# Optimization experiments

Hardware: AMD Instinct MI355X
Metric: run time of the kernel (lower is better)

## Reference

```python
import jax, jax.numpy as jnp
import numpy as np

HEADS = 8
HID = 128
N_A = 10000
N_B = 10000
E = 120000
NG = 8  # graphs in batch
F_A = 256
F_B = 128
NEG_SLOPE = 0.2


def _gat(h_src, h_dst, src, dst, ws, wd, a_s, a_d, bias, num_dst):
    """PyG GATConv, bipartite, concat=False, add_self_loops=False."""
    hs = (h_src @ ws).reshape(-1, HEADS, HID)   # [N_src, H, C]
    hd = (h_dst @ wd).reshape(-1, HEADS, HID)   # [N_dst, H, C]
    al_s = jnp.sum(hs * a_s, axis=-1)           # [N_src, H]
    al_d = jnp.sum(hd * a_d, axis=-1)           # [N_dst, H]
    e = jax.nn.leaky_relu(al_s[src] + al_d[dst], NEG_SLOPE)  # [E, H]
    m = jax.ops.segment_max(e, dst, num_segments=num_dst)
    ex = jnp.exp(e - m[dst])
    denom = jax.ops.segment_sum(ex, dst, num_segments=num_dst)
    alpha = ex / (denom[dst] + 1e-16)           # segment softmax over in-edges
    msg = hs[src] * alpha[:, :, None]           # [E, H, C]
    out = jax.ops.segment_sum(msg, dst, num_segments=num_dst)
    return out.mean(axis=1) + bias              # concat=False -> head mean + bias


def _mean_pool(x, batch, num_graphs):
    s = jax.ops.segment_sum(x, batch, num_segments=num_graphs)
    cnt = jax.ops.segment_sum(jnp.ones((x.shape[0],), x.dtype), batch, num_segments=num_graphs)
    return s / jnp.maximum(cnt, 1.0)[:, None]


def setup_inputs() -> dict:
    key = jax.random.key(0)
    ks = iter(jax.random.split(key, 48))
    rn = lambda shape, s=0.05: jax.random.normal(next(ks), shape, jnp.float32) * s
    inp = {
        'x_a': jax.random.normal(next(ks), (N_A, F_A), jnp.float32),
        'x_b': jax.random.normal(next(ks), (N_B, F_B), jnp.float32),
        'edge_ab': jax.random.randint(next(ks), (2, E), 0, N_A, jnp.int32),
        'edge_ba': jax.random.randint(next(ks), (2, E), 0, N_B, jnp.int32),
        'batch_a': jnp.sort(jax.random.randint(next(ks), (N_A,), 0, NG, jnp.int32)),
        'batch_b': jnp.sort(jax.random.randint(next(ks), (N_B,), 0, NG, jnp.int32)),
        'lin_a_w': rn((F_A, HID)), 'lin_a_b': rn((HID,)),
        'lin_b_w': rn((F_B, HID)), 'lin_b_b': rn((HID,)),
        'fc_w': rn((2 * HID, 1)), 'fc_b': rn((1,)),
    }
    for layer in ('1', '2'):
        for rel in ('ab', 'ba'):
            inp[f'w{layer}s_{rel}'] = rn((HID, HEADS * HID))
            inp[f'w{layer}d_{rel}'] = rn((HID, HEADS * HID))
            inp[f'a{layer}s_{rel}'] = rn((HEADS, HID))
            inp[f'a{layer}d_{rel}'] = rn((HEADS, HID))
            inp[f'b{layer}_{rel}'] = rn((HID,))
    return inp


def reference(x_a, x_b, edge_ab, edge_ba, batch_a, batch_b,
              lin_a_w, lin_a_b, lin_b_w, lin_b_b, fc_w, fc_b,
              w1s_ab, w1d_ab, a1s_ab, a1d_ab, b1_ab,
              w1s_ba, w1d_ba, a1s_ba, a1d_ba, b1_ba,
              w2s_ab, w2d_ab, a2s_ab, a2d_ab, b2_ab,
              w2s_ba, w2d_ba, a2s_ba, a2d_ba, b2_ba):
    ha = jax.nn.relu(x_a @ lin_a_w + lin_a_b)
    hb = jax.nn.relu(x_b @ lin_b_w + lin_b_b)
    # layer 1 (each dst type receives exactly one relation -> HeteroConv mean is identity)
    hb1 = _gat(ha, hb, edge_ab[0], edge_ab[1], w1s_ab, w1d_ab, a1s_ab, a1d_ab, b1_ab, N_B)
    ha1 = _gat(hb, ha, edge_ba[0], edge_ba[1], w1s_ba, w1d_ba, a1s_ba, a1d_ba, b1_ba, N_A)
    ha1 = jax.nn.relu(ha1)
    hb1 = jax.nn.relu(hb1)
    # layer 2
    hb2 = _gat(ha1, hb1, edge_ab[0], edge_ab[1], w2s_ab, w2d_ab, a2s_ab, a2d_ab, b2_ab, N_B)
    ha2 = _gat(hb1, ha1, edge_ba[0], edge_ba[1], w2s_ba, w2d_ba, a2s_ba, a2d_ba, b2_ba, N_A)
    pa = _mean_pool(ha2, batch_a, NG)
    pb = _mean_pool(hb2, batch_b, NG)
    g = jnp.concatenate([pa, pb], axis=1)       # [NG, 2*HID]
    return (g @ fc_w + fc_b).squeeze(-1)        # [NG]
```

## Files before the change

kernel.cpp:

```cpp
#include <hip/hip_runtime.h>
#include <math.h>

#define HID 128
#define HEADS 8

typedef __attribute__((ext_vector_type(8))) short s16x8;
typedef __attribute__((ext_vector_type(4))) float f32x4;

__device__ __forceinline__ unsigned short bf16_rne(float x) {
  unsigned u = __float_as_uint(x);
  unsigned r = u + 0x7FFFu + ((u >> 16) & 1u);
  return (unsigned short)(r >> 16);
}
__device__ __forceinline__ float bf16f(unsigned short h) {
  return __uint_as_float(((unsigned)h) << 16);
}

struct GSeg { const float* A; const float* B; int M; int K; int yb; };

__global__ __launch_bounds__(256, 3) void gemm2_splitk(
    GSeg s0, GSeg s1, float* __restrict__ P, int Mtot, int KS)
{
  __shared__ float As[16][132];
  __shared__ float Bs[16][132];
  const int tid = threadIdx.x;
  const float* A; const float* B; int M, K, rowbase, ytile;
  if ((int)blockIdx.x < s0.yb) {
    A = s0.A; B = s0.B; M = s0.M; K = s0.K; rowbase = 0; ytile = blockIdx.x;
  } else {
    A = s1.A; B = s1.B; M = s1.M; K = s1.K; rowbase = s0.yb * 128; ytile = blockIdx.x - s0.yb;
  }
  const int bm = ytile * 128;
  const int kchunk = K / KS;
  const int kbeg = blockIdx.y * kchunk;

  const int am = tid >> 1;
  const int ak = (tid & 1) << 3;
  const int brr = tid >> 4;
  const int bcc = (tid & 15) << 2;
  const int tx = tid & 15, ty = tid >> 4;

  float acc[64];
#pragma unroll
  for (int i = 0; i < 64; i++) acc[i] = 0.f;

  const int gr = bm + am;
  const float* Arow = A + (size_t)gr * K;
  for (int k0 = kbeg; k0 < kbeg + kchunk; k0 += 16) {
    float4 av0 = make_float4(0.f, 0.f, 0.f, 0.f), av1 = av0;
    if (gr < M) {
      av0 = *(const float4*)(Arow + k0 + ak);
      av1 = *(const float4*)(Arow + k0 + ak + 4);
    }
    const float4 bv0 = *(const float4*)(B + (size_t)(k0 + brr) * HID + bcc);
    const float4 bv1 = *(const float4*)(B + (size_t)(k0 + brr) * HID + bcc + 64);
    As[ak + 0][am] = av0.x; As[ak + 1][am] = av0.y;
    As[ak + 2][am] = av0.z; As[ak + 3][am] = av0.w;
    As[ak + 4][am] = av1.x; As[ak + 5][am] = av1.y;
    As[ak + 6][am] = av1.z; As[ak + 7][am] = av1.w;
    *(float4*)&Bs[brr][bcc] = bv0;
    *(float4*)&Bs[brr][bcc + 64] = bv1;
    __syncthreads();
#pragma unroll
    for (int kk = 0; kk < 16; kk++) {
      const float4 a0 = *(const float4*)&As[kk][ty << 3];
      const float4 a1 = *(const float4*)&As[kk][(ty << 3) + 4];
      const float4 b0 = *(const float4*)&Bs[kk][tx << 3];
      const float4 b1 = *(const float4*)&Bs[kk][(tx << 3) + 4];
      const float ar[8] = {a0.x, a0.y, a0.z, a0.w, a1.x, a1.y, a1.z, a1.w};
      const float bq[8] = {b0.x, b0.y, b0.z, b0.w, b1.x, b1.y, b1.z, b1.w};
#pragma unroll
      for (int i = 0; i < 8; i++)
#pragma unroll
        for (int j = 0; j < 8; j++) acc[i * 8 + j] = fmaf(ar[i], bq[j], acc[i * 8 + j]);
    }
    __syncthreads();
  }
  const size_t prow0 = (size_t)blockIdx.y * Mtot + rowbase + bm;
#pragma unroll
  for (int i = 0; i < 8; i++) {
    float* pp = P + (prow0 + (ty << 3) + i) * HID + (tx << 3);
    *(float4*)pp       = make_float4(acc[i * 8 + 0], acc[i * 8 + 1], acc[i * 8 + 2], acc[i * 8 + 3]);
    *(float4*)(pp + 4) = make_float4(acc[i * 8 + 4], acc[i * 8 + 5], acc[i * 8 + 6], acc[i * 8 + 7]);
  }
}

struct RSeg { float* out; const float* bias; int M; int rowbase; };

__global__ __launch_bounds__(256) void reduce_epi(
    const float* __restrict__ P, int Mtot, int KS, float scale, int do_relu,
    RSeg s0, RSeg s1)
{
  int idx = blockIdx.x * 256 + threadIdx.x;
  if (idx >= Mtot * 32) return;
  int r = idx >> 5;
  int c = (idx & 31) << 2;
  float* outp; const float* bias; int rl;
  if (s1.M > 0 && r >= s1.rowbase) {
    rl = r - s1.rowbase; if (rl >= s1.M) return; outp = s1.out; bias = s1.bias;
  } else {
    rl = r; if (rl >= s0.M) return; outp = s0.out; bias = s0.bias;
  }
  float4 acc = make_float4(0.f, 0.f, 0.f, 0.f);
  for (int z = 0; z < KS; z++) {
    const float4 v = *(const float4*)(P + ((size_t)z * Mtot + r) * HID + c);
    acc.x += v.x; acc.y += v.y; acc.z += v.z; acc.w += v.w;
  }
  const float4 b = *(const float4*)(bias + c);
  acc.x = acc.x * scale + b.x;
  acc.y = acc.y * scale + b.y;
  acc.z = acc.z * scale + b.z;
  acc.w = acc.w * scale + b.w;
  if (do_relu) {
    acc.x = acc.x > 0.f ? acc.x : 0.f;
    acc.y = acc.y > 0.f ? acc.y : 0.f;
    acc.z = acc.z > 0.f ? acc.z : 0.f;
    acc.w = acc.w > 0.f ? acc.w : 0.f;
  }
  *(float4*)(outp + (size_t)rl * HID + c) = acc;
}

struct PrepArgs {
  const float* W[8];
  const float* a[8];
  unsigned short* WThi[4];
  unsigned short* WTlo[4];
  float* v[8];
};

__global__ __launch_bounds__(256) void prep_weights(PrepArgs p)
{
  int bid = blockIdx.x;
  if (bid < 2048) {
    int g = bid >> 9;
    int idx = ((bid & 511) << 8) + threadIdx.x;
    int kidx = idx & 1023;
    int c = idx >> 10;
    int h = kidx >> 7, k = kidx & 127;
    float wv = p.W[2 * g][(size_t)k * (HEADS * HID) + h * HID + c];
    unsigned short hi = bf16_rne(wv);
    unsigned short lo = bf16_rne(wv - bf16f(hi));
    p.WThi[g][idx] = hi;
    p.WTlo[g][idx] = lo;
  } else {
    int u = bid - 2048;
    int wi = u >> 2;
    int gid = ((u & 3) << 8) + threadIdx.x;
    int k = gid >> 3, h = gid & 7;
    const float* wr = p.W[wi] + (size_t)k * (HEADS * HID) + h * HID;
    const float* ar = p.a[wi] + (size_t)h * HID;
    float s = 0.f;
    for (int c = 0; c < HID; c++) s = fmaf(wr[c], ar[c], s);
    p.v[wi][gid] = s;
  }
}

__global__ __launch_bounds__(256) void compute_al4(
    const float* __restrict__ ha, const float* __restrict__ hb,
    const float* __restrict__ v4,
    float* __restrict__ o0, float* __restrict__ o1,
    float* __restrict__ o2, float* __restrict__ o3, int na, int nb)
{
  __shared__ float vsh[4 * HID * HEADS];
  for (int i = threadIdx.x; i < 4 * HID * HEADS; i += 256) vsh[i] = v4[i];
  __syncthreads();
  int gid = blockIdx.x * 256 + threadIdx.x;
  int row = gid >> 3, h = gid & 7;
  const float* hr; float* o; int q, rl;
  if (row < na)                    { q = 0; rl = row;               hr = ha; o = o0; }
  else if (row < na + nb)          { q = 1; rl = row - na;          hr = hb; o = o1; }
  else if (row < na + 2 * nb)      { q = 2; rl = row - na - nb;     hr = hb; o = o2; }
  else if (row < 2 * na + 2 * nb)  { q = 3; rl = row - na - 2 * nb; hr = ha; o = o3; }
  else return;
  hr += (size_t)rl * HID;
  const float* vq = vsh + q * HID * HEADS;
  float s = 0.f;
  for (int k = 0; k < HID; k++) s = fmaf(hr[k], vq[k * HEADS + h], s);
  o[(size_t)rl * HEADS + h] = s;
}

__global__ __launch_bounds__(256) void hist2(
    const int* __restrict__ dst_ab, const int* __restrict__ dst_ba,
    int* __restrict__ cnt_ab, int* __restrict__ cnt_ba, int E)
{
  int gid = blockIdx.x * 256 + threadIdx.x;
  if (gid < E) atomicAdd(&cnt_ab[dst_ab[gid]], 1);
  else if (gid < 2 * E) atomicAdd(&cnt_ba[dst_ba[gid - E]], 1);
}

__global__ __launch_bounds__(1024) void scan2(
    const int* __restrict__ cnt_ab, const int* __restrict__ cnt_ba,
    int* __restrict__ ip_ab, int* __restrict__ ip_ba, int n_ab, int n_ba)
{
  const int* cnt = (blockIdx.x == 0) ? cnt_ab : cnt_ba;
  int* indptr = (blockIdx.x == 0) ? ip_ab : ip_ba;
  int n = (blockIdx.x == 0) ? n_ab : n_ba;
  __shared__ int parts[1024];
  const int tid = threadIdx.x;
  const int base = tid * 10;
  int local[10];
  int s = 0;
#pragma unroll
  for (int j = 0; j < 10; j++) {
    int v = (base + j < n) ? cnt[base + j] : 0;
    local[j] = v; s += v;
  }
  parts[tid] = s;
  __syncthreads();
  for (int off = 1; off < 1024; off <<= 1) {
    int v = (tid >= off) ? parts[tid - off] : 0;
    __syncthreads();
    parts[tid] += v;
    __syncthreads();
  }
  int ex = parts[tid] - s;
#pragma unroll
  for (int j = 0; j < 10; j++) {
    if (base + j < n) indptr[base + j] = ex;
    ex += local[j];
  }
  if (tid == 1023) indptr[n] = parts[1023];
}

__global__ __launch_bounds__(256) void scatter2(
    const int* __restrict__ edge_ab, const int* __restrict__ edge_ba,
    const int* __restrict__ ip_ab, const int* __restrict__ ip_ba,
    int* __restrict__ cur_ab, int* __restrict__ cur_ba,
    int* __restrict__ srcs_ab, int* __restrict__ srcs_ba, int E)
{
  int gid = blockIdx.x * 256 + threadIdx.x;
  if (gid < E) {
    int d = edge_ab[E + gid];
    int pos = ip_ab[d] + atomicAdd(&cur_ab[d], 1);
    srcs_ab[pos] = edge_ab[gid];
  } else if (gid < 2 * E) {
    int g = gid - E;
    int d = edge_ba[E + g];
    int pos = ip_ba[d] + atomicAdd(&cur_ba[d], 1);
    srcs_ba[pos] = edge_ba[g];
  }
}

struct GDir {
  const int* indptr; const int* srcs;
  const float* als; const float* ald;
  const float* h;
  unsigned short* zhi; unsigned short* zlo;
};

__global__ __launch_bounds__(256) void gat_edge2(GDir d0, GDir d1, int n0, int ntot)
{
  const int w = threadIdx.x >> 6;
  const int lane = threadIdx.x & 63;
  const int g = blockIdx.x * 4 + w;
  if (g >= ntot) return;
  const bool first = (g < n0);
  const int n = first ? g : g - n0;
  const int* indptr = first ? d0.indptr : d1.indptr;
  const int* srcs   = first ? d0.srcs   : d1.srcs;
  const float* als  = first ? d0.als    : d1.als;
  const float* ald  = first ? d0.ald    : d1.ald;
  const float* hsrc = first ? d0.h      : d1.h;
  unsigned short* zh = (first ? d0.zhi : d1.zhi) + (size_t)n * (HEADS * HID);
  unsigned short* zl = (first ? d0.zlo : d1.zlo) + (size_t)n * (HEADS * HID);

  const int base = indptr[n];
  const int deg = indptr[n + 1] - base;
  if (deg == 0) {
#pragma unroll
    for (int hh = 0; hh < HEADS; hh++) {
      *(unsigned*)(zh + hh * HID + 2 * lane) = 0u;
      *(unsigned*)(zl + hh * HID + 2 * lane) = 0u;
    }
    return;
  }
  const int eh = lane >> 3, h = lane & 7;
  const float aldn = ald[(size_t)n * HEADS + h];
  const int nch = (deg + 7) >> 3;
  const int ncc = nch < 4 ? nch : 4;

  int sc[4];
  float vc[4];
#pragma unroll
  for (int c = 0; c < 4; c++) {
    int e = c * 8 + eh;
    sc[c] = (c < ncc && e < deg) ? srcs[base + e] : -1;
  }
#pragma unroll
  for (int c = 0; c < 4; c++)
    vc[c] = (sc[c] >= 0) ? als[(size_t)sc[c] * HEADS + h] : 0.f;
  float den = 0.f;
#pragma unroll
  for (int c = 0; c < 4; c++) {
    float v = vc[c] + aldn;
    v = v > 0.f ? v : 0.2f * v;
    float ex = (sc[c] >= 0) ? expf(v) : 0.f;
    vc[c] = ex;
    den += ex;
  }
  for (int e0 = 32; e0 < deg; e0 += 8) {
    int e = e0 + eh;
    if (e < deg) {
      int s = srcs[base + e];
      float v = als[(size_t)s * HEADS + h] + aldn;
      v = v > 0.f ? v : 0.2f * v;
      den += expf(v);
    }
  }
  den += __shfl_xor(den, 8);
  den += __shfl_xor(den, 16);
  den += __shfl_xor(den, 32);

  float acc[16];
#pragma unroll
  for (int i = 0; i < 16; i++) acc[i] = 0.f;
#pragma unroll
  for (int c = 0; c < 4; c++) {
    if (c >= ncc) break;
    const int rem = deg - c * 8;
    const int elim = rem < 8 ? rem : 8;
#pragma unroll
    for (int half = 0; half < 2; half++) {
      if (half * 4 >= elim) break;
      int sj[4];
#pragma unroll
      for (int j = 0; j < 4; j++) {
        int s = __shfl(sc[c], (half * 4 + j) * 8);
        sj[j] = s < 0 ? 0 : s;
      }
      float2 hv[4];
#pragma unroll
      for (int j = 0; j < 4; j++)
        hv[j] = *(const float2*)(hsrc + (size_t)sj[j] * HID + 2 * lane);
#pragma unroll
      for (int j = 0; j < 4; j++) {
#pragma unroll
        for (int hh = 0; hh < 8; hh++) {
          float a = __shfl(vc[c], (half * 4 + j) * 8 + hh);
          acc[2 * hh]     = fmaf(a, hv[j].x, acc[2 * hh]);
          acc[2 * hh + 1] = fmaf(a, hv[j].y, acc[2 * hh + 1]);
        }
      }
    }
  }
  for (int e0 = 32; e0 < deg; e0 += 8) {
    int e = e0 + eh;
    int s = (e < deg) ? srcs[base + e] : -1;
    float ex = 0.f;
    if (s >= 0) {
      float v = als[(size_t)s * HEADS + h] + aldn;
      v = v > 0.f ? v : 0.2f * v;
      ex = expf(v);
    }
    int elim = deg - e0; if (elim > 8) elim = 8;
    for (int e8 = 0; e8 < elim; e8++) {
      int ss = __shfl(s, e8 * 8);
      const float2 hvt = *(const float2*)(hsrc + (size_t)ss * HID + 2 * lane);
#pragma unroll
      for (int hh = 0; hh < 8; hh++) {
        float a = __shfl(ex, e8 * 8 + hh);
        acc[2 * hh]     = fmaf(a, hvt.x, acc[2 * hh]);
        acc[2 * hh + 1] = fmaf(a, hvt.y, acc[2 * hh + 1]);
      }
    }
  }
#pragma unroll
  for (int hh = 0; hh < 8; hh++) {
    float dh = __shfl(den, hh);
    float inv = 1.f / (dh + 1e-16f);
    float x0 = acc[2 * hh] * inv;
    float x1 = acc[2 * hh + 1] * inv;
    unsigned short h0 = bf16_rne(x0), h1 = bf16_rne(x1);
    unsigned short l0 = bf16_rne(x0 - bf16f(h0)), l1 = bf16_rne(x1 - bf16f(h1));
    *(unsigned*)(zh + hh * HID + 2 * lane) = (unsigned)h0 | ((unsigned)h1 << 16);
    *(unsigned*)(zl + hh * HID + 2 * lane) = (unsigned)l0 | ((unsigned)l1 << 16);
  }
}

struct MSeg {
  const unsigned short* Ahi; const unsigned short* Alo;
  const unsigned short* Bhi; const unsigned short* Blo;
  float* out; const float* bias; int M; int yb;
};

__global__ __launch_bounds__(256, 2) void gemm_mfma2(MSeg s0, MSeg s1, float scale, int do_relu)
{
  __shared__ __align__(16) unsigned short smem[12288];
  const int tid = threadIdx.x;
  const unsigned short *Ahi, *Alo, *Bhi, *Blo; const float* bias; float* out; int M, ytile;
  if ((int)blockIdx.x < s0.yb) {
    Ahi = s0.Ahi; Alo = s0.Alo; Bhi = s0.Bhi; Blo = s0.Blo;
    out = s0.out; bias = s0.bias; M = s0.M; ytile = blockIdx.x;
  } else {
    Ahi = s1.Ahi; Alo = s1.Alo; Bhi = s1.Bhi; Blo = s1.Blo;
    out = s1.out; bias = s1.bias; M = s1.M; ytile = blockIdx.x - s0.yb;
  }
  const int bm = ytile * 64;

  const int sr = tid >> 2;
  const int sg = tid & 3;
  const int g1 = sg ^ ((sr >> 1) & 3);
  const int sr2 = sr + 64;
  const int g2 = sg ^ ((sr2 >> 1) & 3);
  const int aslot  = sr * 32 + g1 * 8;
  const int bslotA = sr * 32 + g1 * 8;
  const int bslotB = sr2 * 32 + g2 * 8;
  const unsigned short* gA  = Ahi + (size_t)(bm + sr) * 1024 + sg * 8;
  const unsigned short* gAl = Alo + (size_t)(bm + sr) * 1024 + sg * 8;
  const unsigned short* gB0 = Bhi + (size_t)sr  * 1024 + sg * 8;
  const unsigned short* gB1 = Bhi + (size_t)sr2 * 1024 + sg * 8;
  const unsigned short* gC0 = Blo + (size_t)sr  * 1024 + sg * 8;
  const unsigned short* gC1 = Blo + (size_t)sr2 * 1024 + sg * 8;

  const int l = tid & 63;
  const int w = tid >> 6;
  const int kg = l >> 4;
  int aoff[4], boff[2];
#pragma unroll
  for (int mi = 0; mi < 4; mi++) {
    int r = mi * 16 + (l & 15);
    aoff[mi] = r * 32 + (kg ^ ((r >> 1) & 3)) * 8;
  }
#pragma unroll
  for (int ni = 0; ni < 2; ni++) {
    int r = w * 32 + ni * 16 + (l & 15);
    boff[ni] = r * 32 + (kg ^ ((r >> 1) & 3)) * 8;
  }

  f32x4 acc[4][2];
  const f32x4 z4 = {0.f, 0.f, 0.f, 0.f};
#pragma unroll
  for (int mi = 0; mi < 4; mi++)
#pragma unroll
    for (int ni = 0; ni < 2; ni++) acc[mi][ni] = z4;

  uint4 rA  = *(const uint4*)gA;
  uint4 rAl = *(const uint4*)gAl;
  uint4 rB0 = *(const uint4*)gB0;
  uint4 rB1 = *(const uint4*)gB1;
  uint4 rC0 = *(const uint4*)gC0;
  uint4 rC1 = *(const uint4*)gC1;

  for (int ks = 0; ks < 32; ks++) {
    *(uint4*)&smem[aslot]         = rA;
    *(uint4*)&smem[2048 + aslot]  = rAl;
    *(uint4*)&smem[4096 + bslotA] = rB0;
    *(uint4*)&smem[4096 + bslotB] = rB1;
    *(uint4*)&smem[8192 + bslotA] = rC0;
    *(uint4*)&smem[8192 + bslotB] = rC1;
    __syncthreads();
    if (ks < 31) {
      const int k0 = (ks + 1) * 32;
      rA  = *(const uint4*)(gA  + k0);
      rAl = *(const uint4*)(gAl + k0);
      rB0 = *(const uint4*)(gB0 + k0);
      rB1 = *(const uint4*)(gB1 + k0);
      rC0 = *(const uint4*)(gC0 + k0);
      rC1 = *(const uint4*)(gC1 + k0);
    }
    s16x8 bh0 = *(const s16x8*)&smem[4096 + boff[0]];
    s16x8 bh1 = *(const s16x8*)&smem[4096 + boff[1]];
    s16x8 bl0 = *(const s16x8*)&smem[8192 + boff[0]];
    s16x8 bl1 = *(const s16x8*)&smem[8192 + boff[1]];
#pragma unroll
    for (int mi = 0; mi < 4; mi++) {
      s16x8 ah = *(const s16x8*)&smem[aoff[mi]];
      s16x8 al = *(const s16x8*)&smem[2048 + aoff[mi]];
      acc[mi][0] = __builtin_amdgcn_mfma_f32_16x16x32_bf16(ah, bh0, acc[mi][0], 0, 0, 0);
      acc[mi][1] = __builtin_amdgcn_mfma_f32_16x16x32_bf16(ah, bh1, acc[mi][1], 0, 0, 0);
      acc[mi][0] = __builtin_amdgcn_mfma_f32_16x16x32_bf16(ah, bl0, acc[mi][0], 0, 0, 0);
      acc[mi][1] = __builtin_amdgcn_mfma_f32_16x16x32_bf16(ah, bl1, acc[mi][1], 0, 0, 0);
      acc[mi][0] = __builtin_amdgcn_mfma_f32_16x16x32_bf16(al, bh0, acc[mi][0], 0, 0, 0);
      acc[mi][1] = __builtin_amdgcn_mfma_f32_16x16x32_bf16(al, bh1, acc[mi][1], 0, 0, 0);
      acc[mi][0] = __builtin_amdgcn_mfma_f32_16x16x32_bf16(al, bl0, acc[mi][0], 0, 0, 0);
      acc[mi][1] = __builtin_amdgcn_mfma_f32_16x16x32_bf16(al, bl1, acc[mi][1], 0, 0, 0);
    }
    __syncthreads();
  }

  const int q = l >> 4, cl = l & 15;
#pragma unroll
  for (int ni = 0; ni < 2; ni++) {
    const int col = w * 32 + ni * 16 + cl;
    const float bv = bias[col];
#pragma unroll
    for (int mi = 0; mi < 4; mi++) {
      const int r0 = bm + mi * 16 + q * 4;
      const f32x4 v = acc[mi][ni];
#pragma unroll
      for (int j = 0; j < 4; j++) {
        const int r = r0 + j;
        if (r < M) {
          float x = v[j] * scale + bv;
          if (do_relu) x = fmaxf(x, 0.f);
          out[(size_t)r * HID + col] = x;
        }
      }
    }
  }
}

__global__ __launch_bounds__(256) void pool_dot2(
    const float* __restrict__ ha, const float* __restrict__ hb,
    const int* __restrict__ batch_a, const int* __restrict__ batch_b,
    const float* __restrict__ fc_w, float* __restrict__ gsum, int na, int nb)
{
  const bool isA = blockIdx.x < 160;
  const float* h = isA ? ha : hb;
  const int* batch = isA ? batch_a : batch_b;
  const float* wseg = isA ? fc_w : fc_w + HID;
  float* gs = isA ? gsum : gsum + 8;
  const int n = isA ? na : nb;
  const int b = isA ? blockIdx.x : blockIdx.x - 160;

  __shared__ float sg[8];
  if (threadIdx.x < 8) sg[threadIdx.x] = 0.f;
  __syncthreads();
  const int lane = threadIdx.x & 63;
  const int wv = threadIdx.x >> 6;
  const int gw = b * 4 + wv;
  const int tw = 160 * 4;
  const float2 w2 = *(const float2*)(wseg + lane * 2);
  for (int r = gw; r < n; r += tw) {
    float2 hv = *(const float2*)(h + (size_t)r * HID + lane * 2);
    float s = hv.x * w2.x + hv.y * w2.y;
#pragma unroll
    for (int off = 32; off > 0; off >>= 1) s += __shfl_down(s, off, 64);
    if (lane == 0) atomicAdd(&sg[batch[r]], s);
  }
  __syncthreads();
  if (threadIdx.x < 8) atomicAdd(&gs[threadIdx.x], sg[threadIdx.x]);
}

__global__ __launch_bounds__(64) void finalize_out(
    const float* __restrict__ gsum, const int* __restrict__ batch_a,
    const int* __restrict__ batch_b, const float* __restrict__ fc_b,
    float* __restrict__ out, int na, int nb, int ng)
{
  int g = threadIdx.x;
  if (g >= ng) return;
  int l, r, lo;
  l = 0; r = na; while (l < r) { int m = (l + r) >> 1; if (batch_a[m] < g) l = m + 1; else r = m; } lo = l;
  r = na; while (l < r) { int m = (l + r) >> 1; if (batch_a[m] < g + 1) l = m + 1; else r = m; }
  int ca = l - lo; if (ca < 1) ca = 1;
  l = 0; r = nb; while (l < r) { int m = (l + r) >> 1; if (batch_b[m] < g) l = m + 1; else r = m; } lo = l;
  r = nb; while (l < r) { int m = (l + r) >> 1; if (batch_b[m] < g + 1) l = m + 1; else r = m; }
  int cb = l - lo; if (cb < 1) cb = 1;
  out[g] = gsum[g] / (float)ca + gsum[8 + g] / (float)cb + fc_b[0];
}

extern "C" void kernel_launch(void* const* d_in, const int* in_sizes, int n_in,
                              void* d_out, int out_size, void* d_ws, size_t ws_size,
                              hipStream_t stream)
{
  const float* x_a = (const float*)d_in[0];
  const float* x_b = (const float*)d_in[1];
  const int* edge_ab = (const int*)d_in[2];
  const int* edge_ba = (const int*)d_in[3];
  const int* batch_a = (const int*)d_in[4];
  const int* batch_b = (const int*)d_in[5];
  const float* lin_a_w = (const float*)d_in[6];
  const float* lin_a_b = (const float*)d_in[7];
  const float* lin_b_w = (const float*)d_in[8];
  const float* lin_b_b = (const float*)d_in[9];
  const float* fc_w = (const float*)d_in[10];
  const float* fc_b = (const float*)d_in[11];

  const int NA = in_sizes[4];
  const int NB = in_sizes[5];
  const int E  = in_sizes[2] / 2;
  const int FA = in_sizes[0] / NA;
  const int FB = in_sizes[1] / NB;
  const int NG = out_size;
  const int NMAX = NA > NB ? NA : NB;
  const int NAp = (NA + 127) & ~127, NBp = (NB + 127) & ~127;
  const int NMAXp = NAp > NBp ? NAp : NBp;
  const int yba = NAp / 128, ybb = NBp / 128;
  const int Mtot = NAp + NBp;

  auto al256 = [](size_t b) { return (b + 255) & ~(size_t)255; };
  size_t fixed = 0;
  fixed += 3 * al256((size_t)NAp * HID * 4) + 3 * al256((size_t)NBp * HID * 4);
  fixed += 2 * al256((size_t)NMAXp * 1024 * 2);
  fixed += al256((size_t)8 * 131072 * 2);
  fixed += al256((size_t)8 * HID * HEADS * 4);
  fixed += 2 * al256((size_t)NAp * HEADS * 4) + 2 * al256((size_t)NBp * HEADS * 4);
  fixed += al256(((size_t)4 * NMAX + 16) * 4);
  fixed += al256((size_t)(NB + 1) * 4) + al256((size_t)(NA + 1) * 4);
  fixed += 2 * al256((size_t)E * 4);
  fixed += 8192;
  const size_t zba_sz = 2 * al256((size_t)NAp * 1024 * 2);
  const size_t pslice = al256((size_t)Mtot * HID * 4);

  int KS = 4; bool dual = true;
  if (fixed + zba_sz + 4 * pslice <= ws_size)      { dual = true;  KS = 4; }
  else if (fixed + zba_sz + 2 * pslice <= ws_size) { dual = true;  KS = 2; }
  else if (fixed + 4 * pslice <= ws_size)          { dual = false; KS = 4; }
  else if (fixed + 2 * pslice <= ws_size)          { dual = false; KS = 2; }
  else if (fixed + 1 * pslice <= ws_size)          { dual = false; KS = 1; }
  else return;

  char* w = (char*)d_ws;
  auto carve = [&](size_t bytes) -> void* {
    void* p = (void*)w;
    w += (bytes + 255) & ~(size_t)255;
    return p;
  };
  float* ha0 = (float*)carve((size_t)NAp * HID * 4);
  float* hb0 = (float*)carve((size_t)NBp * HID * 4);
  float* ha1 = (float*)carve((size_t)NAp * HID * 4);
  float* hb1 = (float*)carve((size_t)NBp * HID * 4);
  float* ha2 = (float*)carve((size_t)NAp * HID * 4);
  float* hb2 = (float*)carve((size_t)NBp * HID * 4);
  unsigned short* zab_hi = (unsigned short*)carve((size_t)NMAXp * 1024 * 2);
  unsigned short* zab_lo = (unsigned short*)carve((size_t)NMAXp * 1024 * 2);
  unsigned short* zba_hi = dual ? (unsigned short*)carve((size_t)NAp * 1024 * 2) : zab_hi;
  unsigned short* zba_lo = dual ? (unsigned short*)carve((size_t)NAp * 1024 * 2) : zab_lo;
  float* P   = (float*)carve((size_t)KS * Mtot * HID * 4);
  unsigned short* WT = (unsigned short*)carve((size_t)8 * 131072 * 2);
  float* vv  = (float*)carve((size_t)8 * HID * HEADS * 4);
  float* als_ab = (float*)carve((size_t)NAp * HEADS * 4);
  float* ald_ab = (float*)carve((size_t)NBp * HEADS * 4);
  float* als_ba = (float*)carve((size_t)NBp * HEADS * 4);
  float* ald_ba = (float*)carve((size_t)NAp * HEADS * 4);
  int* csrblk = (int*)carve(((size_t)4 * NMAX + 16) * 4);
  int* indptr_ab = (int*)carve((size_t)(NB + 1) * 4);
  int* indptr_ba = (int*)carve((size_t)(NA + 1) * 4);
  int* srcs_ab   = (int*)carve((size_t)E * 4);
  int* srcs_ba   = (int*)carve((size_t)E * 4);
  if ((size_t)(w - (char*)d_ws) > ws_size) return;

  int* cnt_ab = csrblk;
  int* cnt_ba = csrblk + NMAX;
  int* cur_ab = csrblk + 2 * NMAX;
  int* cur_ba = csrblk + 3 * NMAX;
  float* gsum = (float*)(csrblk + 4 * NMAX);

  hipMemsetAsync(csrblk, 0, ((size_t)4 * NMAX + 16) * 4, stream);

  PrepArgs pa;
  const int wi_idx[8] = {12, 13, 17, 18, 22, 23, 27, 28};
  const int ai_idx[8] = {14, 15, 19, 20, 24, 25, 29, 30};
  for (int i = 0; i < 8; i++) {
    pa.W[i] = (const float*)d_in[wi_idx[i]];
    pa.a[i] = (const float*)d_in[ai_idx[i]];
    pa.v[i] = vv + (size_t)i * HID * HEADS;
  }
  for (int g = 0; g < 4; g++) {
    pa.WThi[g] = WT + (size_t)g * 131072;
    pa.WTlo[g] = WT + (size_t)(4 + g) * 131072;
  }
  prep_weights<<<2048 + 32, 256, 0, stream>>>(pa);

  hist2<<<(2 * E + 255) / 256, 256, 0, stream>>>(edge_ab + E, edge_ba + E, cnt_ab, cnt_ba, E);
  scan2<<<2, 1024, 0, stream>>>(cnt_ab, cnt_ba, indptr_ab, indptr_ba, NB, NA);
  scatter2<<<(2 * E + 255) / 256, 256, 0, stream>>>(
      edge_ab, edge_ba, indptr_ab, indptr_ba, cur_ab, cur_ba, srcs_ab, srcs_ba, E);

  const int red_grid = (Mtot * 32 + 255) / 256;

  {
    GSeg sa = {x_a, lin_a_w, NA, FA, yba};
    GSeg sb = {x_b, lin_b_w, NB, FB, ybb};
    gemm2_splitk<<<dim3(yba + ybb, KS), 256, 0, stream>>>(sa, sb, P, Mtot, KS);
    RSeg ra = {ha0, lin_a_b, NA, 0};
    RSeg rb = {hb0, lin_b_b, NB, yba * 128};
    reduce_epi<<<red_grid, 256, 0, stream>>>(P, Mtot, KS, 1.f, 1, ra, rb);
  }

  auto run_layer = [&](int L, const float* haP, const float* hbP,
                       float* haN, float* hbN, const float* b_ab, const float* b_ba,
                       int relu) {
    compute_al4<<<((2 * (NA + NB)) * HEADS + 255) / 256, 256, 0, stream>>>(
        haP, hbP, vv + (size_t)L * 4 * HID * HEADS,
        als_ab, ald_ab, als_ba, ald_ba, NA, NB);
    GDir dab = {indptr_ab, srcs_ab, als_ab, ald_ab, haP, zab_hi, zab_lo};
    GDir dba = {indptr_ba, srcs_ba, als_ba, ald_ba, hbP, zba_hi, zba_lo};
    const int gab = 2 * L, gba = 2 * L + 1;
    MSeg mab = {zab_hi, zab_lo, WT + (size_t)gab * 131072, WT + (size_t)(4 + gab) * 131072,
                hbN, b_ab, NB, NBp / 64};
    MSeg mba = {zba_hi, zba_lo, WT + (size_t)gba * 131072, WT + (size_t)(4 + gba) * 131072,
                haN, b_ba, NA, NAp / 64};
    if (dual) {
      gat_edge2<<<(NB + NA + 3) / 4, 256, 0, stream>>>(dab, dba, NB, NB + NA);
      gemm_mfma2<<<NBp / 64 + NAp / 64, 256, 0, stream>>>(mab, mba, 1.f / HEADS, relu);
    } else {
      MSeg mz = {nullptr, nullptr, nullptr, nullptr, nullptr, nullptr, 0, 0};
      gat_edge2<<<(NB + 3) / 4, 256, 0, stream>>>(dab, dab, NB, NB);
      gemm_mfma2<<<NBp / 64, 256, 0, stream>>>(mab, mz, 1.f / HEADS, relu);
      gat_edge2<<<(NA + 3) / 4, 256, 0, stream>>>(dba, dba, NA, NA);
      gemm_mfma2<<<NAp / 64, 256, 0, stream>>>(mba, mz, 1.f / HEADS, relu);
    }
  };

  run_layer(0, ha0, hb0, ha1, hb1, (const float*)d_in[16], (const float*)d_in[21], 1);
  run_layer(1, ha1, hb1, ha2, hb2, (const float*)d_in[26], (const float*)d_in[31], 0);

  pool_dot2<<<320, 256, 0, stream>>>(ha2, hb2, batch_a, batch_b, fc_w, gsum, NA, NB);
  finalize_out<<<1, 64, 0, stream>>>(gsum, batch_a, batch_b, fc_b,
                                     (float*)d_out, NA, NB, NG);
}
```

Before: 393.4 us.

## Fuse setup kernels, split MFMA GEMM over K halves, fold finalize into pool

Histogram is merged into the weight-prep kernel, and edge scatter is merged with the input split-K GEMM. Together with folding finalize into the pooling kernel through a last-block ticket, this cuts launch count and lets independent work share the GPU. The layer GEMM now runs 512-thread blocks where each half processes half of K and the halves are combined through shared memory. That doubles waves per tile, at the cost of more LDS and an extra reduction step.

```diff
diff --git a/kernel.cpp b/kernel.cpp
--- a/kernel.cpp
+++ b/kernel.cpp
@@ -14,75 +14,6 @@
 }
 __device__ __forceinline__ float bf16f(unsigned short h) {
   return __uint_as_float(((unsigned)h) << 16);
-}
-
-struct GSeg { const float* A; const float* B; int M; int K; int yb; };
-
-__global__ __launch_bounds__(256, 3) void gemm2_splitk(
-    GSeg s0, GSeg s1, float* __restrict__ P, int Mtot, int KS)
-{
-  __shared__ float As[16][132];
-  __shared__ float Bs[16][132];
-  const int tid = threadIdx.x;
-  const float* A; const float* B; int M, K, rowbase, ytile;
-  if ((int)blockIdx.x < s0.yb) {
-    A = s0.A; B = s0.B; M = s0.M; K = s0.K; rowbase = 0; ytile = blockIdx.x;
-  } else {
-    A = s1.A; B = s1.B; M = s1.M; K = s1.K; rowbase = s0.yb * 128; ytile = blockIdx.x - s0.yb;
-  }
-  const int bm = ytile * 128;
-  const int kchunk = K / KS;
-  const int kbeg = blockIdx.y * kchunk;
-
-  const int am = tid >> 1;
-  const int ak = (tid & 1) << 3;
-  const int brr = tid >> 4;
-  const int bcc = (tid & 15) << 2;
-  const int tx = tid & 15, ty = tid >> 4;
-
-  float acc[64];
-#pragma unroll
-  for (int i = 0; i < 64; i++) acc[i] = 0.f;
-
-  const int gr = bm + am;
-  const float* Arow = A + (size_t)gr * K;
-  for (int k0 = kbeg; k0 < kbeg + kchunk; k0 += 16) {
-    float4 av0 = make_float4(0.f, 0.f, 0.f, 0.f), av1 = av0;
-    if (gr < M) {
-      av0 = *(const float4*)(Arow + k0 + ak);
-      av1 = *(const float4*)(Arow + k0 + ak + 4);
-    }
-    const float4 bv0 = *(const float4*)(B + (size_t)(k0 + brr) * HID + bcc);
-    const float4 bv1 = *(const float4*)(B + (size_t)(k0 + brr) * HID + bcc + 64);
-    As[ak + 0][am] = av0.x; As[ak + 1][am] = av0.y;
-    As[ak + 2][am] = av0.z; As[ak + 3][am] = av0.w;
-    As[ak + 4][am] = av1.x; As[ak + 5][am] = av1.y;
-    As[ak + 6][am] = av1.z; As[ak + 7][am] = av1.w;
-    *(float4*)&Bs[brr][bcc] = bv0;
-    *(float4*)&Bs[brr][bcc + 64] = bv1;
-    __syncthreads();
-#pragma unroll
-    for (int kk = 0; kk < 16; kk++) {
-      const float4 a0 = *(const float4*)&As[kk][ty << 3];
-      const float4 a1 = *(const float4*)&As[kk][(ty << 3) + 4];
-      const float4 b0 = *(const float4*)&Bs[kk][tx << 3];
-      const float4 b1 = *(const float4*)&Bs[kk][(tx << 3) + 4];
-      const float ar[8] = {a0.x, a0.y, a0.z, a0.w, a1.x, a1.y, a1.z, a1.w};
-      const float bq[8] = {b0.x, b0.y, b0.z, b0.w, b1.x, b1.y, b1.z, b1.w};
-#pragma unroll
-      for (int i = 0; i < 8; i++)
-#pragma unroll
-        for (int j = 0; j < 8; j++) acc[i * 8 + j] = fmaf(ar[i], bq[j], acc[i * 8 + j]);
-    }
-    __syncthreads();
-  }
-  const size_t prow0 = (size_t)blockIdx.y * Mtot + rowbase + bm;
-#pragma unroll
-  for (int i = 0; i < 8; i++) {
-    float* pp = P + (prow0 + (ty << 3) + i) * HID + (tx << 3);
-    *(float4*)pp       = make_float4(acc[i * 8 + 0], acc[i * 8 + 1], acc[i * 8 + 2], acc[i * 8 + 3]);
-    *(float4*)(pp + 4) = make_float4(acc[i * 8 + 4], acc[i * 8 + 5], acc[i * 8 + 6], acc[i * 8 + 7]);
-  }
 }
 
 struct RSeg { float* out; const float* bias; int M; int rowbase; };
@@ -128,7 +59,9 @@
   float* v[8];
 };
 
-__global__ __launch_bounds__(256) void prep_weights(PrepArgs p)
+__global__ __launch_bounds__(256) void prep_hist(
+    PrepArgs p, const int* __restrict__ dst_ab, const int* __restrict__ dst_ba,
+    int* __restrict__ cnt_ab, int* __restrict__ cnt_ba, int E)
 {
   int bid = blockIdx.x;
   if (bid < 2048) {
@@ -142,7 +75,7 @@
     unsigned short lo = bf16_rne(wv - bf16f(hi));
     p.WThi[g][idx] = hi;
     p.WTlo[g][idx] = lo;
-  } else {
+  } else if (bid < 2080) {
     int u = bid - 2048;
     int wi = u >> 2;
     int gid = ((u & 3) << 8) + threadIdx.x;
@@ -152,6 +85,137 @@
     float s = 0.f;
     for (int c = 0; c < HID; c++) s = fmaf(wr[c], ar[c], s);
     p.v[wi][gid] = s;
+  } else {
+    int gid = (bid - 2080) * 256 + threadIdx.x;
+    if (gid < E) atomicAdd(&cnt_ab[dst_ab[gid]], 1);
+    else if (gid < 2 * E) atomicAdd(&cnt_ba[dst_ba[gid - E]], 1);
+  }
+}
+
+__global__ __launch_bounds__(1024) void scan2(
+    const int* __restrict__ cnt_ab, const int* __restrict__ cnt_ba,
+    int* __restrict__ ip_ab, int* __restrict__ ip_ba, int n_ab, int n_ba)
+{
+  const int* cnt = (blockIdx.x == 0) ? cnt_ab : cnt_ba;
+  int* indptr = (blockIdx.x == 0) ? ip_ab : ip_ba;
+  int n = (blockIdx.x == 0) ? n_ab : n_ba;
+  __shared__ int parts[1024];
+  const int tid = threadIdx.x;
+  const int base = tid * 10;
+  int local[10];
+  int s = 0;
+#pragma unroll
+  for (int j = 0; j < 10; j++) {
+    int v = (base + j < n) ? cnt[base + j] : 0;
+    local[j] = v; s += v;
+  }
+  parts[tid] = s;
+  __syncthreads();
+  for (int off = 1; off < 1024; off <<= 1) {
+    int v = (tid >= off) ? parts[tid - off] : 0;
+    __syncthreads();
+    parts[tid] += v;
+    __syncthreads();
+  }
+  int ex = parts[tid] - s;
+#pragma unroll
+  for (int j = 0; j < 10; j++) {
+    if (base + j < n) indptr[base + j] = ex;
+    ex += local[j];
+  }
+  if (tid == 1023) indptr[n] = parts[1023];
+}
+
+struct GSeg { const float* A; const float* B; int M; int K; int yb; };
+
+__global__ __launch_bounds__(256, 3) void scatter_gemm_in(
+    const int* __restrict__ edge_ab, const int* __restrict__ edge_ba,
+    const int* __restrict__ ip_ab, const int* __restrict__ ip_ba,
+    int* __restrict__ cur_ab, int* __restrict__ cur_ba,
+    int* __restrict__ srcs_ab, int* __restrict__ srcs_ba, int E, int scat_b,
+    GSeg s0, GSeg s1, float* __restrict__ P, int Mtot, int KS)
+{
+  __shared__ float As[16][132];
+  __shared__ float Bs[16][132];
+  const int bid0 = blockIdx.x;
+  if (bid0 < scat_b) {
+    int gid = bid0 * 256 + threadIdx.x;
+    if (gid < E) {
+      int d = edge_ab[E + gid];
+      int pos = ip_ab[d] + atomicAdd(&cur_ab[d], 1);
+      srcs_ab[pos] = edge_ab[gid];
+    } else if (gid < 2 * E) {
+      int g = gid - E;
+      int d = edge_ba[E + g];
+      int pos = ip_ba[d] + atomicAdd(&cur_ba[d], 1);
+      srcs_ba[pos] = edge_ba[g];
+    }
+    return;
+  }
+  const int gg = bid0 - scat_b;
+  const int nxt = s0.yb + s1.yb;
+  const int bx = gg % nxt;
+  const int by = gg / nxt;
+
+  const int tid = threadIdx.x;
+  const float* A; const float* B; int M, K, rowbase, ytile;
+  if (bx < s0.yb) {
+    A = s0.A; B = s0.B; M = s0.M; K = s0.K; rowbase = 0; ytile = bx;
+  } else {
+    A = s1.A; B = s1.B; M = s1.M; K = s1.K; rowbase = s0.yb * 128; ytile = bx - s0.yb;
+  }
+  const int bm = ytile * 128;
+  const int kchunk = K / KS;
+  const int kbeg = by * kchunk;
+
+  const int am = tid >> 1;
+  const int ak = (tid & 1) << 3;
+  const int brr = tid >> 4;
+  const int bcc = (tid & 15) << 2;
+  const int tx = tid & 15, ty = tid >> 4;
+
+  float acc[64];
+#pragma unroll
+  for (int i = 0; i < 64; i++) acc[i] = 0.f;
+
+  const int gr = bm + am;
+  const float* Arow = A + (size_t)gr * K;
+  for (int k0 = kbeg; k0 < kbeg + kchunk; k0 += 16) {
+    float4 av0 = make_float4(0.f, 0.f, 0.f, 0.f), av1 = av0;
+    if (gr < M) {
+      av0 = *(const float4*)(Arow + k0 + ak);
+      av1 = *(const float4*)(Arow + k0 + ak + 4);
+    }
+    const float4 bv0 = *(const float4*)(B + (size_t)(k0 + brr) * HID + bcc);
+    const float4 bv1 = *(const float4*)(B + (size_t)(k0 + brr) * HID + bcc + 64);
+    As[ak + 0][am] = av0.x; As[ak + 1][am] = av0.y;
+    As[ak + 2][am] = av0.z; As[ak + 3][am] = av0.w;
+    As[ak + 4][am] = av1.x; As[ak + 5][am] = av1.y;
+    As[ak + 6][am] = av1.z; As[ak + 7][am] = av1.w;
+    *(float4*)&Bs[brr][bcc] = bv0;
+    *(float4*)&Bs[brr][bcc + 64] = bv1;
+    __syncthreads();
+#pragma unroll
+    for (int kk = 0; kk < 16; kk++) {
+      const float4 a0 = *(const float4*)&As[kk][ty << 3];
+      const float4 a1 = *(const float4*)&As[kk][(ty << 3) + 4];
+      const float4 b0 = *(const float4*)&Bs[kk][tx << 3];
+      const float4 b1 = *(const float4*)&Bs[kk][(tx << 3) + 4];
+      const float ar[8] = {a0.x, a0.y, a0.z, a0.w, a1.x, a1.y, a1.z, a1.w};
+      const float bq[8] = {b0.x, b0.y, b0.z, b0.w, b1.x, b1.y, b1.z, b1.w};
+#pragma unroll
+      for (int i = 0; i < 8; i++)
+#pragma unroll
+        for (int j = 0; j < 8; j++) acc[i * 8 + j] = fmaf(ar[i], bq[j], acc[i * 8 + j]);
+    }
+    __syncthreads();
+  }
+  const size_t prow0 = (size_t)by * Mtot + rowbase + bm;
+#pragma unroll
+  for (int i = 0; i < 8; i++) {
+    float* pp = P + (prow0 + (ty << 3) + i) * HID + (tx << 3);
+    *(float4*)pp       = make_float4(acc[i * 8 + 0], acc[i * 8 + 1], acc[i * 8 + 2], acc[i * 8 + 3]);
+    *(float4*)(pp + 4) = make_float4(acc[i * 8 + 4], acc[i * 8 + 5], acc[i * 8 + 6], acc[i * 8 + 7]);
   }
 }
 
@@ -179,68 +243,6 @@
   o[(size_t)rl * HEADS + h] = s;
 }
 
-__global__ __launch_bounds__(256) void hist2(
-    const int* __restrict__ dst_ab, const int* __restrict__ dst_ba,
-    int* __restrict__ cnt_ab, int* __restrict__ cnt_ba, int E)
-{
-  int gid = blockIdx.x * 256 + threadIdx.x;
-  if (gid < E) atomicAdd(&cnt_ab[dst_ab[gid]], 1);
-  else if (gid < 2 * E) atomicAdd(&cnt_ba[dst_ba[gid - E]], 1);
-}
-
-__global__ __launch_bounds__(1024) void scan2(
-    const int* __restrict__ cnt_ab, const int* __restrict__ cnt_ba,
-    int* __restrict__ ip_ab, int* __restrict__ ip_ba, int n_ab, int n_ba)
-{
-  const int* cnt = (blockIdx.x == 0) ? cnt_ab : cnt_ba;
-  int* indptr = (blockIdx.x == 0) ? ip_ab : ip_ba;
-  int n = (blockIdx.x == 0) ? n_ab : n_ba;
-  __shared__ int parts[1024];
-  const int tid = threadIdx.x;
-  const int base = tid * 10;
-  int local[10];
-  int s = 0;
-#pragma unroll
-  for (int j = 0; j < 10; j++) {
-    int v = (base + j < n) ? cnt[base + j] : 0;
-    local[j] = v; s += v;
-  }
-  parts[tid] = s;
-  __syncthreads();
-  for (int off = 1; off < 1024; off <<= 1) {
-    int v = (tid >= off) ? parts[tid - off] : 0;
-    __syncthreads();
-    parts[tid] += v;
-    __syncthreads();
-  }
-  int ex = parts[tid] - s;
-#pragma unroll
-  for (int j = 0; j < 10; j++) {
-    if (base + j < n) indptr[base + j] = ex;
-    ex += local[j];
-  }
-  if (tid == 1023) indptr[n] = parts[1023];
-}
-
-__global__ __launch_bounds__(256) void scatter2(
-    const int* __restrict__ edge_ab, const int* __restrict__ edge_ba,
-    const int* __restrict__ ip_ab, const int* __restrict__ ip_ba,
-    int* __restrict__ cur_ab, int* __restrict__ cur_ba,
-    int* __restrict__ srcs_ab, int* __restrict__ srcs_ba, int E)
-{
-  int gid = blockIdx.x * 256 + threadIdx.x;
-  if (gid < E) {
-    int d = edge_ab[E + gid];
-    int pos = ip_ab[d] + atomicAdd(&cur_ab[d], 1);
-    srcs_ab[pos] = edge_ab[gid];
-  } else if (gid < 2 * E) {
-    int g = gid - E;
-    int d = edge_ba[E + g];
-    int pos = ip_ba[d] + atomicAdd(&cur_ba[d], 1);
-    srcs_ba[pos] = edge_ba[g];
-  }
-}
-
 struct GDir {
   const int* indptr; const int* srcs;
   const float* als; const float* ald;
@@ -383,9 +385,9 @@
   float* out; const float* bias; int M; int yb;
 };
 
-__global__ __launch_bounds__(256, 2) void gemm_mfma2(MSeg s0, MSeg s1, float scale, int do_relu)
-{
-  __shared__ __align__(16) unsigned short smem[12288];
+__global__ __launch_bounds__(512) void gemm_mfma8(MSeg s0, MSeg s1, float scale, int do_relu)
+{
+  __shared__ __align__(16) unsigned short smem[24576];
   const int tid = threadIdx.x;
   const unsigned short *Ahi, *Alo, *Bhi, *Blo; const float* bias; float* out; int M, ytile;
   if ((int)blockIdx.x < s0.yb) {
@@ -396,24 +398,28 @@
     out = s1.out; bias = s1.bias; M = s1.M; ytile = blockIdx.x - s0.yb;
   }
   const int bm = ytile * 64;
-
-  const int sr = tid >> 2;
-  const int sg = tid & 3;
+  const int half = tid >> 8;
+  const int t = tid & 255;
+  const int kbase = half * 512;
+  unsigned short* sm = smem + half * 12288;
+
+  const int sr = t >> 2;
+  const int sg = t & 3;
   const int g1 = sg ^ ((sr >> 1) & 3);
   const int sr2 = sr + 64;
   const int g2 = sg ^ ((sr2 >> 1) & 3);
   const int aslot  = sr * 32 + g1 * 8;
   const int bslotA = sr * 32 + g1 * 8;
   const int bslotB = sr2 * 32 + g2 * 8;
-  const unsigned short* gA  = Ahi + (size_t)(bm + sr) * 1024 + sg * 8;
-  const unsigned short* gAl = Alo + (size_t)(bm + sr) * 1024 + sg * 8;
-  const unsigned short* gB0 = Bhi + (size_t)sr  * 1024 + sg * 8;
-  const unsigned short* gB1 = Bhi + (size_t)sr2 * 1024 + sg * 8;
-  const unsigned short* gC0 = Blo + (size_t)sr  * 1024 + sg * 8;
-  const unsigned short* gC1 = Blo + (size_t)sr2 * 1024 + sg * 8;
-
-  const int l = tid & 63;
-  const int w = tid >> 6;
+  const unsigned short* gA  = Ahi + (size_t)(bm + sr) * 1024 + kbase + sg * 8;
+  const unsigned short* gAl = Alo + (size_t)(bm + sr) * 1024 + kbase + sg * 8;
+  const unsigned short* gB0 = Bhi + (size_t)sr  * 1024 + kbase + sg * 8;
+  const unsigned short* gB1 = Bhi + (size_t)sr2 * 1024 + kbase + sg * 8;
+  const unsigned short* gC0 = Blo + (size_t)sr  * 1024 + kbase + sg * 8;
+  const unsigned short* gC1 = Blo + (size_t)sr2 * 1024 + kbase + sg * 8;
+
+  const int l = t & 63;
+  const int w = t >> 6;
   const int kg = l >> 4;
   int aoff[4], boff[2];
 #pragma unroll
@@ -441,15 +447,15 @@
   uint4 rC0 = *(const uint4*)gC0;
   uint4 rC1 = *(const uint4*)gC1;
 
-  for (int ks = 0; ks < 32; ks++) {
-    *(uint4*)&smem[aslot]         = rA;
-    *(uint4*)&smem[2048 + aslot]  = rAl;
-    *(uint4*)&smem[4096 + bslotA] = rB0;
-    *(uint4*)&smem[4096 + bslotB] = rB1;
-    *(uint4*)&smem[8192 + bslotA] = rC0;
-    *(uint4*)&smem[8192 + bslotB] = rC1;
+  for (int ks = 0; ks < 16; ks++) {
+    *(uint4*)&sm[aslot]         = rA;
+    *(uint4*)&sm[2048 + aslot]  = rAl;
+    *(uint4*)&sm[4096 + bslotA] = rB0;
+    *(uint4*)&sm[4096 + bslotB] = rB1;
+    *(uint4*)&sm[8192 + bslotA] = rC0;
+    *(uint4*)&sm[8192 + bslotB] = rC1;
     __syncthreads();
-    if (ks < 31) {
+    if (ks < 15) {
       const int k0 = (ks + 1) * 32;
       rA  = *(const uint4*)(gA  + k0);
       rAl = *(const uint4*)(gAl + k0);
@@ -458,14 +464,14 @@
       rC0 = *(const uint4*)(gC0 + k0);
       rC1 = *(const uint4*)(gC1 + k0);
     }
-    s16x8 bh0 = *(const s16x8*)&smem[4096 + boff[0]];
-    s16x8 bh1 = *(const s16x8*)&smem[4096 + boff[1]];
-    s16x8 bl0 = *(const s16x8*)&smem[8192 + boff[0]];
-    s16x8 bl1 = *(const s16x8*)&smem[8192 + boff[1]];
+    s16x8 bh0 = *(const s16x8*)&sm[4096 + boff[0]];
+    s16x8 bh1 = *(const s16x8*)&sm[4096 + boff[1]];
+    s16x8 bl0 = *(const s16x8*)&sm[8192 + boff[0]];
+    s16x8 bl1 = *(const s16x8*)&sm[8192 + boff[1]];
 #pragma unroll
     for (int mi = 0; mi < 4; mi++) {
-      s16x8 ah = *(const s16x8*)&smem[aoff[mi]];
-      s16x8 al = *(const s16x8*)&smem[2048 + aoff[mi]];
+      s16x8 ah = *(const s16x8*)&sm[aoff[mi]];
+      s16x8 al = *(const s16x8*)&sm[2048 + aoff[mi]];
       acc[mi][0] = __builtin_amdgcn_mfma_f32_16x16x32_bf16(ah, bh0, acc[mi][0], 0, 0, 0);
       acc[mi][1] = __builtin_amdgcn_mfma_f32_16x16x32_bf16(ah, bh1, acc[mi][1], 0, 0, 0);
       acc[mi][0] = __builtin_amdgcn_mfma_f32_16x16x32_bf16(ah, bl0, acc[mi][0], 0, 0, 0);
@@ -478,32 +484,51 @@
     __syncthreads();
   }
 
+  float* fred = (float*)smem;
   const int q = l >> 4, cl = l & 15;
-#pragma unroll
-  for (int ni = 0; ni < 2; ni++) {
-    const int col = w * 32 + ni * 16 + cl;
-    const float bv = bias[col];
-#pragma unroll
-    for (int mi = 0; mi < 4; mi++) {
-      const int r0 = bm + mi * 16 + q * 4;
-      const f32x4 v = acc[mi][ni];
-#pragma unroll
-      for (int j = 0; j < 4; j++) {
-        const int r = r0 + j;
-        if (r < M) {
-          float x = v[j] * scale + bv;
-          if (do_relu) x = fmaxf(x, 0.f);
-          out[(size_t)r * HID + col] = x;
+  if (half == 1) {
+#pragma unroll
+    for (int ni = 0; ni < 2; ni++) {
+      const int col = w * 32 + ni * 16 + cl;
+#pragma unroll
+      for (int mi = 0; mi < 4; mi++) {
+        const f32x4 v = acc[mi][ni];
+#pragma unroll
+        for (int j = 0; j < 4; j++)
+          fred[(mi * 16 + q * 4 + j) * 128 + col] = v[j];
+      }
+    }
+  }
+  __syncthreads();
+  if (half == 0) {
+#pragma unroll
+    for (int ni = 0; ni < 2; ni++) {
+      const int col = w * 32 + ni * 16 + cl;
+      const float bv = bias[col];
+#pragma unroll
+      for (int mi = 0; mi < 4; mi++) {
+        const int rt = mi * 16 + q * 4;
+        const f32x4 v = acc[mi][ni];
+#pragma unroll
+        for (int j = 0; j < 4; j++) {
+          const int r = bm + rt + j;
+          if (r < M) {
+            float x = (v[j] + fred[(rt + j) * 128 + col]) * scale + bv;
+            if (do_relu) x = fmaxf(x, 0.f);
+            out[(size_t)r * HID + col] = x;
+          }
         }
       }
     }
   }
 }
 
-__global__ __launch_bounds__(256) void pool_dot2(
+__global__ __launch_bounds__(256) void pool_fin(
     const float* __restrict__ ha, const float* __restrict__ hb,
     const int* __restrict__ batch_a, const int* __restrict__ batch_b,
-    const float* __restrict__ fc_w, float* __restrict__ gsum, int na, int nb)
+    const float* __restrict__ fc_w, const float* __restrict__ fc_b,
+    float* __restrict__ gsum, int* __restrict__ ticket,
+    float* __restrict__ out, int na, int nb, int ng)
 {
   const bool isA = blockIdx.x < 160;
   const float* h = isA ? ha : hb;
@@ -514,6 +539,7 @@
   const int b = isA ? blockIdx.x : blockIdx.x - 160;
 
   __shared__ float sg[8];
+  __shared__ int lastf;
   if (threadIdx.x < 8) sg[threadIdx.x] = 0.f;
   __syncthreads();
   const int lane = threadIdx.x & 63;
@@ -530,23 +556,27 @@
   }
   __syncthreads();
   if (threadIdx.x < 8) atomicAdd(&gs[threadIdx.x], sg[threadIdx.x]);
-}
-
-__global__ __launch_bounds__(64) void finalize_out(
-    const float* __restrict__ gsum, const int* __restrict__ batch_a,
-    const int* __restrict__ batch_b, const float* __restrict__ fc_b,
-    float* __restrict__ out, int na, int nb, int ng)
-{
-  int g = threadIdx.x;
-  if (g >= ng) return;
-  int l, r, lo;
-  l = 0; r = na; while (l < r) { int m = (l + r) >> 1; if (batch_a[m] < g) l = m + 1; else r = m; } lo = l;
-  r = na; while (l < r) { int m = (l + r) >> 1; if (batch_a[m] < g + 1) l = m + 1; else r = m; }
-  int ca = l - lo; if (ca < 1) ca = 1;
-  l = 0; r = nb; while (l < r) { int m = (l + r) >> 1; if (batch_b[m] < g) l = m + 1; else r = m; } lo = l;
-  r = nb; while (l < r) { int m = (l + r) >> 1; if (batch_b[m] < g + 1) l = m + 1; else r = m; }
-  int cb = l - lo; if (cb < 1) cb = 1;
-  out[g] = gsum[g] / (float)ca + gsum[8 + g] / (float)cb + fc_b[0];
+  if (threadIdx.x == 0) {
+    __threadfence();
+    int tk = atomicAdd(ticket, 1);
+    lastf = (tk == (int)gridDim.x - 1);
+  }
+  __syncthreads();
+  if (lastf) {
+    int g = threadIdx.x;
+    if (g < ng) {
+      int l, r, lo;
+      l = 0; r = na; while (l < r) { int m = (l + r) >> 1; if (batch_a[m] < g) l = m + 1; else r = m; } lo = l;
+      r = na; while (l < r) { int m = (l + r) >> 1; if (batch_a[m] < g + 1) l = m + 1; else r = m; }
+      int ca = l - lo; if (ca < 1) ca = 1;
+      l = 0; r = nb; while (l < r) { int m = (l + r) >> 1; if (batch_b[m] < g) l = m + 1; else r = m; } lo = l;
+      r = nb; while (l < r) { int m = (l + r) >> 1; if (batch_b[m] < g + 1) l = m + 1; else r = m; }
+      int cb = l - lo; if (cb < 1) cb = 1;
+      float va = atomicAdd(&gsum[g], 0.f);
+      float vb = atomicAdd(&gsum[8 + g], 0.f);
+      out[g] = va / (float)ca + vb / (float)cb + fc_b[0];
+    }
+  }
 }
 
 extern "C" void kernel_launch(void* const* d_in, const int* in_sizes, int n_in,
@@ -585,7 +615,7 @@
   fixed += al256((size_t)8 * 131072 * 2);
   fixed += al256((size_t)8 * HID * HEADS * 4);
   fixed += 2 * al256((size_t)NAp * HEADS * 4) + 2 * al256((size_t)NBp * HEADS * 4);
-  fixed += al256(((size_t)4 * NMAX + 16) * 4);
+  fixed += al256(((size_t)4 * NMAX + 24) * 4);
   fixed += al256((size_t)(NB + 1) * 4) + al256((size_t)(NA + 1) * 4);
   fixed += 2 * al256((size_t)E * 4);
   fixed += 8192;
@@ -623,7 +653,7 @@
   float* ald_ab = (float*)carve((size_t)NBp * HEADS * 4);
   float* als_ba = (float*)carve((size_t)NBp * HEADS * 4);
   float* ald_ba = (float*)carve((size_t)NAp * HEADS * 4);
-  int* csrblk = (int*)carve(((size_t)4 * NMAX + 16) * 4);
+  int* csrblk = (int*)carve(((size_t)4 * NMAX + 24) * 4);
   int* indptr_ab = (int*)carve((size_t)(NB + 1) * 4);
   int* indptr_ba = (int*)carve((size_t)(NA + 1) * 4);
   int* srcs_ab   = (int*)carve((size_t)E * 4);
@@ -635,8 +665,9 @@
   int* cur_ab = csrblk + 2 * NMAX;
   int* cur_ba = csrblk + 3 * NMAX;
   float* gsum = (float*)(csrblk + 4 * NMAX);
-
-  hipMemsetAsync(csrblk, 0, ((size_t)4 * NMAX + 16) * 4, stream);
+  int* ticket = csrblk + 4 * NMAX + 16;
+
+  hipMemsetAsync(csrblk, 0, ((size_t)4 * NMAX + 24) * 4, stream);
 
   PrepArgs pa;
   const int wi_idx[8] = {12, 13, 17, 18, 22, 23, 27, 28};
@@ -650,22 +681,21 @@
     pa.WThi[g] = WT + (size_t)g * 131072;
     pa.WTlo[g] = WT + (size_t)(4 + g) * 131072;
   }
-  prep_weights<<<2048 + 32, 256, 0, stream>>>(pa);
-
-  hist2<<<(2 * E + 255) / 256, 256, 0, stream>>>(edge_ab + E, edge_ba + E, cnt_ab, cnt_ba, E);
+  const int hist_b = (2 * E + 255) / 256;
+  prep_hist<<<2080 + hist_b, 256, 0, stream>>>(pa, edge_ab + E, edge_ba + E,
+                                               cnt_ab, cnt_ba, E);
   scan2<<<2, 1024, 0, stream>>>(cnt_ab, cnt_ba, indptr_ab, indptr_ba, NB, NA);
-  scatter2<<<(2 * E + 255) / 256, 256, 0, stream>>>(
-      edge_ab, edge_ba, indptr_ab, indptr_ba, cur_ab, cur_ba, srcs_ab, srcs_ba, E);
-
-  const int red_grid = (Mtot * 32 + 255) / 256;
 
   {
     GSeg sa = {x_a, lin_a_w, NA, FA, yba};
     GSeg sb = {x_b, lin_b_w, NB, FB, ybb};
-    gemm2_splitk<<<dim3(yba + ybb, KS), 256, 0, stream>>>(sa, sb, P, Mtot, KS);
+    const int scat_b = (2 * E + 255) / 256;
+    scatter_gemm_in<<<scat_b + (yba + ybb) * KS, 256, 0, stream>>>(
+        edge_ab, edge_ba, indptr_ab, indptr_ba, cur_ab, cur_ba,
+        srcs_ab, srcs_ba, E, scat_b, sa, sb, P, Mtot, KS);
     RSeg ra = {ha0, lin_a_b, NA, 0};
     RSeg rb = {hb0, lin_b_b, NB, yba * 128};
-    reduce_epi<<<red_grid, 256, 0, stream>>>(P, Mtot, KS, 1.f, 1, ra, rb);
+    reduce_epi<<<(Mtot * 32 + 255) / 256, 256, 0, stream>>>(P, Mtot, KS, 1.f, 1, ra, rb);
   }
 
   auto run_layer = [&](int L, const float* haP, const float* hbP,
@@ -683,20 +713,19 @@
                 haN, b_ba, NA, NAp / 64};
     if (dual) {
       gat_edge2<<<(NB + NA + 3) / 4, 256, 0, stream>>>(dab, dba, NB, NB + NA);
-      gemm_mfma2<<<NBp / 64 + NAp / 64, 256, 0, stream>>>(mab, mba, 1.f / HEADS, relu);
+      gemm_mfma8<<<NBp / 64 + NAp / 64, 512, 0, stream>>>(mab, mba, 1.f / HEADS, relu);
     } else {
       MSeg mz = {nullptr, nullptr, nullptr, nullptr, nullptr, nullptr, 0, 0};
       gat_edge2<<<(NB + 3) / 4, 256, 0, stream>>>(dab, dab, NB, NB);
-      gemm_mfma2<<<NBp / 64, 256, 0, stream>>>(mab, mz, 1.f / HEADS, relu);
+      gemm_mfma8<<<NBp / 64, 512, 0, stream>>>(mab, mz, 1.f / HEADS, relu);
       gat_edge2<<<(NA + 3) / 4, 256, 0, stream>>>(dba, dba, NA, NA);
-      gemm_mfma2<<<NAp / 64, 256, 0, stream>>>(mba, mz, 1.f / HEADS, relu);
+      gemm_mfma8<<<NAp / 64, 512, 0, stream>>>(mba, mz, 1.f / HEADS, relu);
     }
   };
 
   run_layer(0, ha0, hb0, ha1, hb1, (const float*)d_in[16], (const float*)d_in[21], 1);
   run_layer(1, ha1, hb1, ha2, hb2, (const float*)d_in[26], (const float*)d_in[31], 0);
 
-  pool_dot2<<<320, 256, 0, stream>>>(ha2, hb2, batch_a, batch_b, fc_w, gsum, NA, NB);
-  finalize_out<<<1, 64, 0, stream>>>(gsum, batch_a, batch_b, fc_b,
-                                     (float*)d_out, NA, NB, NG);
-}
+  pool_fin<<<320, 256, 0, stream>>>(ha2, hb2, batch_a, batch_b, fc_w, fc_b,
+                                    gsum, ticket, (float*)d_out, NA, NB, NG);
+}
```

Measured after the change: 391.2 us. No clear change (-0.6%).
